# Optimization experiments

Hardware: AMD Instinct MI355X
Metric: run time of the kernel (lower is better)

Reference implementation:

```python
import jax, jax.numpy as jnp
import numpy as np

N, K, D = 131072, 4096, 64


def setup_inputs() -> dict:
    key = jax.random.key(0)
    k1, k2 = jax.random.split(key)
    z_e_x = jax.random.normal(k1, (N, D), dtype=jnp.float32)
    codebook = jax.random.normal(k2, (K, D), dtype=jnp.float32)
    return {"z_e_x": z_e_x, "codebook": codebook}


def reference(z_e_x, codebook):
    inputs_sqr = jnp.sum(z_e_x * z_e_x, axis=1, keepdims=True)       # [N, 1]
    codebook_sqr = jnp.sum(codebook * codebook, axis=1)              # [K]
    distances = inputs_sqr + codebook_sqr - 2.0 * jnp.einsum(
        'nd,kd->nk', z_e_x, codebook)                                # [N, K]
    indices = jnp.argmin(distances, axis=1)                          # [N]
    codes = jnp.take(codebook, indices, axis=0)                      # [N, D]
    # Straight-through path: grads pass to z_e_x, not to codebook
    z_q_x_st = z_e_x + jax.lax.stop_gradient(codes - z_e_x)
    # Differentiable-codebook path (index_select on live weight)
    z_q_x_bar = codes
    return jnp.stack([z_q_x_st, z_q_x_bar])                          # [2, N, D]
```

## Files before the change

### kernel.cpp

```cpp
#include <hip/hip_runtime.h>

typedef __attribute__((ext_vector_type(8))) short short8;
typedef __attribute__((ext_vector_type(4))) float f32x4;

constexpr int N_ROWS = 131072;
constexpr int K_CB   = 4096;
constexpr int D_DIM  = 64;
constexpr float EPS_MARGIN = 2.5e-3f;

constexpr size_t CTR_OFF   = 0;
constexpr size_t CSQ_OFF   = 64;
constexpr size_t CBH_OFF   = 16512;
constexpr size_t CBL_OFF   = CBH_OFF + 524288;
constexpr size_t LIST_OFF  = CBL_OFF + 524288;

#define MFMA(a, b, c) __builtin_amdgcn_mfma_f32_16x16x32_bf16((a), (b), (c), 0, 0, 0)

__device__ __forceinline__ unsigned short f2bf(float f) {
    unsigned int u = __builtin_bit_cast(unsigned int, f);
    u = (u + 0x7fffu + ((u >> 16) & 1u)) >> 16;
    return (unsigned short)u;
}
__device__ __forceinline__ float bf2f(unsigned short h) {
    return __builtin_bit_cast(float, ((unsigned int)h) << 16);
}

__device__ __forceinline__ short8 ldfrag(const unsigned char* smbase, int row, int lane, int ks) {
    const int slot = (((lane >> 4) + ks * 4) ^ (lane & 7));
    uint4 v = *(const uint4*)(smbase + row * 128 + slot * 16);
    return __builtin_bit_cast(short8, v);
}

__global__ __launch_bounds__(256)
void prep_csq(const float* __restrict__ cb, float* __restrict__ csq) {
    const int k = blockIdx.x * 256 + threadIdx.x;
    const float4* row = (const float4*)(cb + (size_t)k * D_DIM);
    float s = 0.f;
    #pragma unroll
    for (int i = 0; i < 16; ++i) {
        float4 v = row[i];
        s = fmaf(v.x, v.x, s); s = fmaf(v.y, v.y, s);
        s = fmaf(v.z, v.z, s); s = fmaf(v.w, v.w, s);
    }
    csq[k] = s;
}

__global__ __launch_bounds__(256)
void prep_split(const float* __restrict__ cb, unsigned char* __restrict__ cbh,
                unsigned char* __restrict__ cbl) {
    const int id  = blockIdx.x * 256 + threadIdx.x;
    const int row = id >> 3, s = id & 7;
    const float4* src = (const float4*)(cb + (size_t)row * D_DIM + s * 8);
    float4 v0 = src[0], v1 = src[1];
    float f[8] = {v0.x, v0.y, v0.z, v0.w, v1.x, v1.y, v1.z, v1.w};
    unsigned int hw[4], lw[4];
    #pragma unroll
    for (int i = 0; i < 4; ++i) {
        unsigned short h0 = f2bf(f[2*i]),     l0 = f2bf(f[2*i]     - bf2f(h0));
        unsigned short h1 = f2bf(f[2*i + 1]), l1 = f2bf(f[2*i + 1] - bf2f(h1));
        hw[i] = (unsigned int)h0 | ((unsigned int)h1 << 16);
        lw[i] = (unsigned int)l0 | ((unsigned int)l1 << 16);
    }
    const int slot = s ^ (row & 7);
    *(uint4*)(cbh + (size_t)row * 128 + slot * 16) = make_uint4(hw[0], hw[1], hw[2], hw[3]);
    *(uint4*)(cbl + (size_t)row * 128 + slot * 16) = make_uint4(lw[0], lw[1], lw[2], lw[3]);
}

__global__ void init_counter(int* counter) { if (threadIdx.x == 0) *counter = 0; }

__device__ __forceinline__ void stage_tile(const unsigned char* __restrict__ cbh,
                                           const unsigned char* __restrict__ cbl,
                                           const float* __restrict__ csqg,
                                           unsigned char* sm, int kt, int wid, int lane) {
    const unsigned char* sh = cbh + (size_t)kt * 128;
    const unsigned char* sl = cbl + (size_t)kt * 128;
    #pragma unroll
    for (int p = 0; p < 2; ++p) {
        const int chunk = wid * 2 + p;
        __builtin_amdgcn_global_load_lds(
            (const __attribute__((address_space(1))) void*)(sh + chunk * 1024 + lane * 16),
            (__attribute__((address_space(3))) void*)(sm + chunk * 1024), 16, 0, 0);
    }
    #pragma unroll
    for (int p = 0; p < 2; ++p) {
        const int chunk = wid * 2 + p;
        __builtin_amdgcn_global_load_lds(
            (const __attribute__((address_space(1))) void*)(sl + chunk * 1024 + lane * 16),
            (__attribute__((address_space(3))) void*)(sm + 8192 + chunk * 1024), 16, 0, 0);
    }
    if (wid == 0) {
        __builtin_amdgcn_global_load_lds(
            (const __attribute__((address_space(1))) void*)(csqg + kt + lane),
            (__attribute__((address_space(3))) void*)(sm + 16384), 4, 0, 0);
    }
}

__global__ __launch_bounds__(256, 4)
void vq_main_mfma(const float* __restrict__ z,
                  const float* __restrict__ cb,
                  const unsigned char* __restrict__ cbh,
                  const unsigned char* __restrict__ cbl,
                  const float* __restrict__ csqg,
                  int* __restrict__ list,
                  int* __restrict__ counter, float* __restrict__ out) {
    __shared__ __align__(16) unsigned char sm[2][16640];
    unsigned char* smf = &sm[0][0];
    const int t = threadIdx.x, lane = t & 63, wid = t >> 6;
    const int n0 = blockIdx.x * 128;
    const int wbase = wid * 32;

    #pragma unroll
    for (int p = 0; p < 4; ++p) {
        const int id = t + p * 256;
        const int row = id >> 3, s = id & 7;
        const float4* src = (const float4*)(z + (size_t)(n0 + row) * D_DIM + s * 8);
        float4 v0 = src[0], v1 = src[1];
        float f[8] = {v0.x, v0.y, v0.z, v0.w, v1.x, v1.y, v1.z, v1.w};
        unsigned int hw[4], lw[4];
        #pragma unroll
        for (int i = 0; i < 4; ++i) {
            unsigned short h0 = f2bf(f[2*i]),     l0 = f2bf(f[2*i]     - bf2f(h0));
            unsigned short h1 = f2bf(f[2*i + 1]), l1 = f2bf(f[2*i + 1] - bf2f(h1));
            hw[i] = (unsigned int)h0 | ((unsigned int)h1 << 16);
            lw[i] = (unsigned int)l0 | ((unsigned int)l1 << 16);
        }
        const int slot = s ^ (row & 7);
        *(uint4*)(smf + row * 128 + slot * 16)         = make_uint4(hw[0], hw[1], hw[2], hw[3]);
        *(uint4*)(smf + 16384 + row * 128 + slot * 16) = make_uint4(lw[0], lw[1], lw[2], lw[3]);
    }
    __syncthreads();

    short8 ah[2][2], al[2][2];
    #pragma unroll
    for (int m = 0; m < 2; ++m)
        #pragma unroll
        for (int ks = 0; ks < 2; ++ks) {
            const int row = wbase + m * 16 + (lane & 15);
            ah[m][ks] = ldfrag(smf,         row, lane, ks);
            al[m][ks] = ldfrag(smf + 16384, row, lane, ks);
        }
    __syncthreads();

    float b1[2][4], b2[2][4]; int i1[2][4];
    #pragma unroll
    for (int m = 0; m < 2; ++m)
        #pragma unroll
        for (int r = 0; r < 4; ++r) { b1[m][r] = __builtin_inff(); b2[m][r] = __builtin_inff(); i1[m][r] = 0; }

    stage_tile(cbh, cbl, csqg, &sm[0][0], 0, wid, lane);
    __syncthreads();
    int cur = 0;
    for (int kt = 0; kt < K_CB; kt += 64) {
        if (kt + 64 < K_CB)
            stage_tile(cbh, cbl, csqg, &sm[cur ^ 1][0], kt + 64, wid, lane);
        const unsigned char* bhp = &sm[cur][0];
        const unsigned char* blp = &sm[cur][8192];
        const float* cs_l = (const float*)&sm[cur][16384];
        #pragma unroll 2
        for (int c = 0; c < 4; ++c) {
            const int brow = c * 16 + (lane & 15);
            short8 bh0 = ldfrag(bhp, brow, lane, 0), bh1 = ldfrag(bhp, brow, lane, 1);
            short8 bl0 = ldfrag(blp, brow, lane, 0), bl1 = ldfrag(blp, brow, lane, 1);
            const float cs = cs_l[c * 16 + (lane & 15)];
            const int idx = kt + c * 16 + (lane & 15);
            #pragma unroll
            for (int m = 0; m < 2; ++m) {
                f32x4 a0 = {0.f, 0.f, 0.f, 0.f}, a1 = {0.f, 0.f, 0.f, 0.f};
                a0 = MFMA(ah[m][0], bh0, a0);
                a1 = MFMA(ah[m][1], bh1, a1);
                a0 = MFMA(al[m][0], bh0, a0);
                a1 = MFMA(al[m][1], bh1, a1);
                a0 = MFMA(ah[m][0], bl0, a0);
                a1 = MFMA(ah[m][1], bl1, a1);
                #pragma unroll
                for (int r = 0; r < 4; ++r) {
                    const float d = fmaf(a0[r] + a1[r], -2.f, cs);
                    const bool lt = d < b1[m][r];
                    b2[m][r] = fminf(b2[m][r], lt ? b1[m][r] : d);
                    b1[m][r] = lt ? d : b1[m][r];
                    i1[m][r] = lt ? idx : i1[m][r];
                }
            }
        }
        __syncthreads();
        cur ^= 1;
    }

    int* bidx_lds = (int*)&sm[0][0];
    #pragma unroll
    for (int m = 0; m < 2; ++m)
        #pragma unroll
        for (int r = 0; r < 4; ++r) {
            float v1 = b1[m][r], v2 = b2[m][r]; int j1 = i1[m][r];
            #pragma unroll
            for (int msk = 1; msk < 16; msk <<= 1) {
                const float ov1 = __shfl_xor(v1, msk);
                const int   oj1 = __shfl_xor(j1, msk);
                const float ov2 = __shfl_xor(v2, msk);
                const bool take = (ov1 < v1) || (ov1 == v1 && oj1 < j1);
                const float nv2 = fminf(take ? v1 : v2, take ? ov2 : ov1);
                v1 = take ? ov1 : v1; j1 = take ? oj1 : j1; v2 = nv2;
            }
            if ((lane & 15) == 0) {
                const int rloc = wbase + m * 16 + (lane >> 4) * 4 + r;
                bidx_lds[rloc] = j1;
                if (v2 - v1 < EPS_MARGIN) {
                    const int p = atomicAdd(counter, 1);
                    list[p] = n0 + rloc;
                }
            }
        }
    __syncthreads();

    const float4* cb4 = (const float4*)cb;
    float4* out4 = (float4*)out;
    #pragma unroll
    for (int p = 0; p < 8; ++p) {
        const int id  = t + p * 256;
        const int row = id >> 4, c4 = id & 15;
        const int k = bidx_lds[row];
        const float4 v = cb4[(size_t)k * 16 + c4];
        out4[(size_t)(n0 + row) * 16 + c4] = v;
        out4[(size_t)N_ROWS * 16 + (size_t)(n0 + row) * 16 + c4] = v;
    }
}

__global__ __launch_bounds__(256)
void repair_kernel(const float* __restrict__ z, const float* __restrict__ cb,
                   const float* __restrict__ csq, const int* __restrict__ list,
                   const int* __restrict__ counter, float* __restrict__ out) {
    __shared__ float xs[64];
    __shared__ float rv[4];
    __shared__ int   ri[4];
    __shared__ int   fi_s;
    const int cnt = counter[0];
    const int t = threadIdx.x;
    for (int e = blockIdx.x; e < cnt; e += gridDim.x) {
        const int row = list[e];
        __syncthreads();
        if (t < 64) xs[t] = z[(size_t)row * D_DIM + t];
        __syncthreads();
        float bv = __builtin_inff(); int bi = 0x7fffffff;
        for (int k = t; k < K_CB; k += 256) {
            const float4* cr = (const float4*)(cb + (size_t)k * D_DIM);
            float dot = 0.f;
            #pragma unroll
            for (int i = 0; i < 16; ++i) {
                float4 v = cr[i];
                dot = fmaf(v.x, xs[i * 4 + 0], dot);
                dot = fmaf(v.y, xs[i * 4 + 1], dot);
                dot = fmaf(v.z, xs[i * 4 + 2], dot);
                dot = fmaf(v.w, xs[i * 4 + 3], dot);
            }
            const float d = fmaf(dot, -2.f, csq[k]);
            if (d < bv) { bv = d; bi = k; }
        }
        #pragma unroll
        for (int msk = 1; msk < 64; msk <<= 1) {
            const float ov = __shfl_xor(bv, msk);
            const int   oi = __shfl_xor(bi, msk);
            if (ov < bv || (ov == bv && oi < bi)) { bv = ov; bi = oi; }
        }
        if ((t & 63) == 0) { rv[t >> 6] = bv; ri[t >> 6] = bi; }
        __syncthreads();
        if (t == 0) {
            float fb = rv[0]; int fi = ri[0];
            #pragma unroll
            for (int w = 1; w < 4; ++w)
                if (rv[w] < fb || (rv[w] == fb && ri[w] < fi)) { fb = rv[w]; fi = ri[w]; }
            fi_s = fi;
        }
        __syncthreads();
        if (t < 32) {
            const int dest = t >> 4, c4 = t & 15;
            const float4 v = ((const float4*)cb)[(size_t)fi_s * 16 + c4];
            float4* dst = (float4*)out + (size_t)dest * N_ROWS * 16 + (size_t)row * 16 + c4;
            *dst = v;
        }
        __syncthreads();
    }
}

extern "C" void kernel_launch(void* const* d_in, const int* in_sizes, int n_in,
                              void* d_out, int out_size, void* d_ws, size_t ws_size,
                              hipStream_t stream) {
    const float* z  = (const float*)d_in[0];
    const float* cb = (const float*)d_in[1];
    float* out = (float*)d_out;
    unsigned char* ws = (unsigned char*)d_ws;

    int*   counter = (int*)(ws + CTR_OFF);
    float* csq     = (float*)(ws + CSQ_OFF);
    unsigned char* cbh = ws + CBH_OFF;
    unsigned char* cbl = ws + CBL_OFF;
    int* list  = (int*)(ws + LIST_OFF);

    prep_csq<<<K_CB / 256, 256, 0, stream>>>(cb, csq);
    prep_split<<<(K_CB * 8) / 256, 256, 0, stream>>>(cb, cbh, cbl);
    init_counter<<<1, 64, 0, stream>>>(counter);
    vq_main_mfma<<<N_ROWS / 128, 256, 0, stream>>>(z, cb, cbh, cbl, csq, list, counter, out);
    repair_kernel<<<1024, 256, 0, stream>>>(z, cb, csq, list, counter, out);
}
```

Measured before the change: 255.9 us.

## Switch distance GEMM to 32x32x16 MFMA with bias-initialized accumulator argmax

Replaces the 16x16x32 bf16 MFMA tiling with 32x32x16 MFMA, so each wave computes a 32x32 tile per codebook subtile. The accumulator is pre-seeded with -0.5*|c|^2 (stored replicated as float4 per code), which turns the argmin into an argmax of x·c - 0.5|c|^2 and removes the per-element fma. This cuts MFMA issue count and LDS fragment loads per output and removes the epilogue arithmetic. In exchange it uses more accumulator and tracking registers (16 per lane for each of best, second-best and index), which may pressure occupancy at launch bounds 4.

```diff
diff --git a/kernel.cpp b/kernel.cpp
--- a/kernel.cpp
+++ b/kernel.cpp
@@ -1,7 +1,8 @@
 #include <hip/hip_runtime.h>
 
-typedef __attribute__((ext_vector_type(8))) short short8;
-typedef __attribute__((ext_vector_type(4))) float f32x4;
+typedef __attribute__((ext_vector_type(8)))  short short8;
+typedef __attribute__((ext_vector_type(4)))  float f32x4;
+typedef __attribute__((ext_vector_type(16))) float f32x16;
 
 constexpr int N_ROWS = 131072;
 constexpr int K_CB   = 4096;
@@ -10,11 +11,14 @@
 
 constexpr size_t CTR_OFF   = 0;
 constexpr size_t CSQ_OFF   = 64;
-constexpr size_t CBH_OFF   = 16512;
+constexpr size_t NCSQ4_OFF = CSQ_OFF + 16384;
+constexpr size_t CBH_OFF   = NCSQ4_OFF + 65536;
 constexpr size_t CBL_OFF   = CBH_OFF + 524288;
 constexpr size_t LIST_OFF  = CBL_OFF + 524288;
 
-#define MFMA(a, b, c) __builtin_amdgcn_mfma_f32_16x16x32_bf16((a), (b), (c), 0, 0, 0)
+#define MFMA32(a, b, c) __builtin_amdgcn_mfma_f32_32x32x16_bf16((a), (b), (c), 0, 0, 0)
+
+union Acc16 { f32x16 v; f32x4 q[4]; };
 
 __device__ __forceinline__ unsigned short f2bf(float f) {
     unsigned int u = __builtin_bit_cast(unsigned int, f);
@@ -25,14 +29,15 @@
     return __builtin_bit_cast(float, ((unsigned int)h) << 16);
 }
 
-__device__ __forceinline__ short8 ldfrag(const unsigned char* smbase, int row, int lane, int ks) {
-    const int slot = (((lane >> 4) + ks * 4) ^ (lane & 7));
-    uint4 v = *(const uint4*)(smbase + row * 128 + slot * 16);
+__device__ __forceinline__ short8 ldfrag32(const unsigned char* base, int row, int g, int ks) {
+    const int slot = ((2 * ks + g) ^ (row & 7));
+    uint4 v = *(const uint4*)(base + row * 128 + slot * 16);
     return __builtin_bit_cast(short8, v);
 }
 
 __global__ __launch_bounds__(256)
-void prep_csq(const float* __restrict__ cb, float* __restrict__ csq) {
+void prep_csq(const float* __restrict__ cb, float* __restrict__ csq,
+              float4* __restrict__ ncsq4) {
     const int k = blockIdx.x * 256 + threadIdx.x;
     const float4* row = (const float4*)(cb + (size_t)k * D_DIM);
     float s = 0.f;
@@ -43,6 +48,8 @@
         s = fmaf(v.z, v.z, s); s = fmaf(v.w, v.w, s);
     }
     csq[k] = s;
+    const float n = -0.5f * s;
+    ncsq4[k] = make_float4(n, n, n, n);
 }
 
 __global__ __launch_bounds__(256)
@@ -70,7 +77,7 @@
 
 __device__ __forceinline__ void stage_tile(const unsigned char* __restrict__ cbh,
                                            const unsigned char* __restrict__ cbl,
-                                           const float* __restrict__ csqg,
+                                           const float* __restrict__ ncsq4,
                                            unsigned char* sm, int kt, int wid, int lane) {
     const unsigned char* sh = cbh + (size_t)kt * 128;
     const unsigned char* sl = cbl + (size_t)kt * 128;
@@ -80,18 +87,15 @@
         __builtin_amdgcn_global_load_lds(
             (const __attribute__((address_space(1))) void*)(sh + chunk * 1024 + lane * 16),
             (__attribute__((address_space(3))) void*)(sm + chunk * 1024), 16, 0, 0);
-    }
-    #pragma unroll
-    for (int p = 0; p < 2; ++p) {
-        const int chunk = wid * 2 + p;
         __builtin_amdgcn_global_load_lds(
             (const __attribute__((address_space(1))) void*)(sl + chunk * 1024 + lane * 16),
             (__attribute__((address_space(3))) void*)(sm + 8192 + chunk * 1024), 16, 0, 0);
     }
     if (wid == 0) {
         __builtin_amdgcn_global_load_lds(
-            (const __attribute__((address_space(1))) void*)(csqg + kt + lane),
-            (__attribute__((address_space(3))) void*)(sm + 16384), 4, 0, 0);
+            (const __attribute__((address_space(1))) void*)
+                ((const unsigned char*)ncsq4 + (size_t)kt * 16 + lane * 16),
+            (__attribute__((address_space(3))) void*)(sm + 16384), 16, 0, 0);
     }
 }
 
@@ -100,12 +104,13 @@
                   const float* __restrict__ cb,
                   const unsigned char* __restrict__ cbh,
                   const unsigned char* __restrict__ cbl,
-                  const float* __restrict__ csqg,
+                  const float* __restrict__ ncsq4,
                   int* __restrict__ list,
                   int* __restrict__ counter, float* __restrict__ out) {
-    __shared__ __align__(16) unsigned char sm[2][16640];
+    __shared__ __align__(16) unsigned char sm[2][17408];
     unsigned char* smf = &sm[0][0];
     const int t = threadIdx.x, lane = t & 63, wid = t >> 6;
+    const int g = lane >> 5, colv = lane & 31;
     const int n0 = blockIdx.x * 128;
     const int wbase = wid * 32;
 
@@ -130,57 +135,61 @@
     }
     __syncthreads();
 
-    short8 ah[2][2], al[2][2];
-    #pragma unroll
-    for (int m = 0; m < 2; ++m)
-        #pragma unroll
-        for (int ks = 0; ks < 2; ++ks) {
-            const int row = wbase + m * 16 + (lane & 15);
-            ah[m][ks] = ldfrag(smf,         row, lane, ks);
-            al[m][ks] = ldfrag(smf + 16384, row, lane, ks);
-        }
+    short8 ah[4], al[4];
+    {
+        const int arow = wbase + colv;
+        #pragma unroll
+        for (int ks = 0; ks < 4; ++ks) {
+            ah[ks] = ldfrag32(smf,         arow, g, ks);
+            al[ks] = ldfrag32(smf + 16384, arow, g, ks);
+        }
+    }
     __syncthreads();
 
-    float b1[2][4], b2[2][4]; int i1[2][4];
-    #pragma unroll
-    for (int m = 0; m < 2; ++m)
-        #pragma unroll
-        for (int r = 0; r < 4; ++r) { b1[m][r] = __builtin_inff(); b2[m][r] = __builtin_inff(); i1[m][r] = 0; }
-
-    stage_tile(cbh, cbl, csqg, &sm[0][0], 0, wid, lane);
+    float b1[16], b2[16]; int i1[16];
+    #pragma unroll
+    for (int j = 0; j < 16; ++j) {
+        b1[j] = -__builtin_inff(); b2[j] = -__builtin_inff(); i1[j] = 0;
+    }
+
+    stage_tile(cbh, cbl, ncsq4, &sm[0][0], 0, wid, lane);
     __syncthreads();
     int cur = 0;
     for (int kt = 0; kt < K_CB; kt += 64) {
         if (kt + 64 < K_CB)
-            stage_tile(cbh, cbl, csqg, &sm[cur ^ 1][0], kt + 64, wid, lane);
+            stage_tile(cbh, cbl, ncsq4, &sm[cur ^ 1][0], kt + 64, wid, lane);
         const unsigned char* bhp = &sm[cur][0];
         const unsigned char* blp = &sm[cur][8192];
-        const float* cs_l = (const float*)&sm[cur][16384];
-        #pragma unroll 2
-        for (int c = 0; c < 4; ++c) {
-            const int brow = c * 16 + (lane & 15);
-            short8 bh0 = ldfrag(bhp, brow, lane, 0), bh1 = ldfrag(bhp, brow, lane, 1);
-            short8 bl0 = ldfrag(blp, brow, lane, 0), bl1 = ldfrag(blp, brow, lane, 1);
-            const float cs = cs_l[c * 16 + (lane & 15)];
-            const int idx = kt + c * 16 + (lane & 15);
-            #pragma unroll
-            for (int m = 0; m < 2; ++m) {
-                f32x4 a0 = {0.f, 0.f, 0.f, 0.f}, a1 = {0.f, 0.f, 0.f, 0.f};
-                a0 = MFMA(ah[m][0], bh0, a0);
-                a1 = MFMA(ah[m][1], bh1, a1);
-                a0 = MFMA(al[m][0], bh0, a0);
-                a1 = MFMA(al[m][1], bh1, a1);
-                a0 = MFMA(ah[m][0], bl0, a0);
-                a1 = MFMA(ah[m][1], bl1, a1);
-                #pragma unroll
-                for (int r = 0; r < 4; ++r) {
-                    const float d = fmaf(a0[r] + a1[r], -2.f, cs);
-                    const bool lt = d < b1[m][r];
-                    b2[m][r] = fminf(b2[m][r], lt ? b1[m][r] : d);
-                    b1[m][r] = lt ? d : b1[m][r];
-                    i1[m][r] = lt ? idx : i1[m][r];
-                }
+        const unsigned char* ncs_l = &sm[cur][16384];
+        #pragma unroll
+        for (int ct = 0; ct < 2; ++ct) {
+            const int cidx = ct * 32 + colv;
+            short8 bh[4], bl[4];
+            #pragma unroll
+            for (int ks = 0; ks < 4; ++ks) {
+                bh[ks] = ldfrag32(bhp, cidx, g, ks);
+                bl[ks] = ldfrag32(blp, cidx, g, ks);
             }
+            Acc16 ac;
+            const f32x4* ncsp = (const f32x4*)(ncs_l + cidx * 16);
+            #pragma unroll
+            for (int q = 0; q < 4; ++q) ac.q[q] = *ncsp;
+            f32x16 acc = ac.v;
+            #pragma unroll
+            for (int ks = 0; ks < 4; ++ks) acc = MFMA32(ah[ks], bh[ks], acc);
+            #pragma unroll
+            for (int ks = 0; ks < 4; ++ks) acc = MFMA32(al[ks], bh[ks], acc);
+            #pragma unroll
+            for (int ks = 0; ks < 4; ++ks) acc = MFMA32(ah[ks], bl[ks], acc);
+            const int idx = kt + cidx;
+            #pragma unroll
+            for (int j = 0; j < 16; ++j) {
+                const float m = acc[j];
+                const bool gt = m > b1[j];
+                b2[j] = fmaxf(b2[j], gt ? b1[j] : m);
+                b1[j] = gt ? m : b1[j];
+                i1[j] = gt ? idx : i1[j];
+            }
         }
         __syncthreads();
         cur ^= 1;
@@ -188,28 +197,26 @@
 
     int* bidx_lds = (int*)&sm[0][0];
     #pragma unroll
-    for (int m = 0; m < 2; ++m)
-        #pragma unroll
-        for (int r = 0; r < 4; ++r) {
-            float v1 = b1[m][r], v2 = b2[m][r]; int j1 = i1[m][r];
-            #pragma unroll
-            for (int msk = 1; msk < 16; msk <<= 1) {
-                const float ov1 = __shfl_xor(v1, msk);
-                const int   oj1 = __shfl_xor(j1, msk);
-                const float ov2 = __shfl_xor(v2, msk);
-                const bool take = (ov1 < v1) || (ov1 == v1 && oj1 < j1);
-                const float nv2 = fminf(take ? v1 : v2, take ? ov2 : ov1);
-                v1 = take ? ov1 : v1; j1 = take ? oj1 : j1; v2 = nv2;
+    for (int j = 0; j < 16; ++j) {
+        float v1 = b1[j], v2 = b2[j]; int j1 = i1[j];
+        #pragma unroll
+        for (int msk = 1; msk < 32; msk <<= 1) {
+            const float ov1 = __shfl_xor(v1, msk);
+            const int   oj1 = __shfl_xor(j1, msk);
+            const float ov2 = __shfl_xor(v2, msk);
+            const bool take = (ov1 > v1) || (ov1 == v1 && oj1 < j1);
+            const float nv2 = fmaxf(take ? v1 : v2, take ? ov2 : ov1);
+            v1 = take ? ov1 : v1; j1 = take ? oj1 : j1; v2 = nv2;
+        }
+        if ((lane & 31) == 0) {
+            const int rloc = wbase + (j & 3) + 8 * (j >> 2) + 4 * g;
+            bidx_lds[rloc] = j1;
+            if (2.0f * (v1 - v2) < EPS_MARGIN) {
+                const int p = atomicAdd(counter, 1);
+                list[p] = n0 + rloc;
             }
-            if ((lane & 15) == 0) {
-                const int rloc = wbase + m * 16 + (lane >> 4) * 4 + r;
-                bidx_lds[rloc] = j1;
-                if (v2 - v1 < EPS_MARGIN) {
-                    const int p = atomicAdd(counter, 1);
-                    list[p] = n0 + rloc;
-                }
-            }
-        }
+        }
+    }
     __syncthreads();
 
     const float4* cb4 = (const float4*)cb;
@@ -289,15 +296,17 @@
     float* out = (float*)d_out;
     unsigned char* ws = (unsigned char*)d_ws;
 
-    int*   counter = (int*)(ws + CTR_OFF);
-    float* csq     = (float*)(ws + CSQ_OFF);
+    int*    counter = (int*)(ws + CTR_OFF);
+    float*  csq     = (float*)(ws + CSQ_OFF);
+    float4* ncsq4   = (float4*)(ws + NCSQ4_OFF);
     unsigned char* cbh = ws + CBH_OFF;
     unsigned char* cbl = ws + CBL_OFF;
     int* list  = (int*)(ws + LIST_OFF);
 
-    prep_csq<<<K_CB / 256, 256, 0, stream>>>(cb, csq);
+    prep_csq<<<K_CB / 256, 256, 0, stream>>>(cb, csq, ncsq4);
     prep_split<<<(K_CB * 8) / 256, 256, 0, stream>>>(cb, cbh, cbl);
     init_counter<<<1, 64, 0, stream>>>(counter);
-    vq_main_mfma<<<N_ROWS / 128, 256, 0, stream>>>(z, cb, cbh, cbl, csq, list, counter, out);
+    vq_main_mfma<<<N_ROWS / 128, 256, 0, stream>>>(z, cb, cbh, cbl, (const float*)ncsq4,
+                                                   list, counter, out);
     repair_kernel<<<1024, 256, 0, stream>>>(z, cb, csq, list, counter, out);
 }
```

After: 831.8 us. 3.25x slower.
